# Kernel tuning notes

Measured on AMD Instinct MI355X. Metric: run time of the kernel, lower is better.

The kernel has to match this reference:

```python
import jax, jax.numpy as jnp
import numpy as np

NTYPES = 4
RCUT = 6.0
MIXED_TYPES = False
BOX = 40.0  # Angstrom, sets realistic atomic density


def setup_inputs() -> dict:
    key = jax.random.key(0)
    k1, k2 = jax.random.split(key)
    nframes, nloc = 2, 4096
    coord = jax.random.uniform(k1, (nframes, nloc * 3), dtype=jnp.float32) * BOX
    atype = jax.random.randint(k2, (nframes, nloc), 0, NTYPES, dtype=jnp.int32)
    return {"coord": coord, "atype": atype}


def reference(coord, atype):
    # cell=None branch: extended coords == local coords, nall == nloc
    nframes = coord.shape[0]
    c = coord.reshape(nframes, -1, 3)              # (f, nloc, 3)
    nloc = c.shape[1]
    # diff[f, i, j] = coord[j] - coord[i], shape (f, nloc, nall, 3)
    diff = c[:, None, :, :] - c[:, :, None, :]
    rr2 = jnp.sum(diff * diff, axis=-1)            # (f, nloc, nall)
    # mask self-pairs with inf (torch sets diff rows to inf before squaring)
    eye = jnp.eye(nloc, dtype=bool)
    rr2 = jnp.where(eye[None, :, :], jnp.inf, rr2)
    min_rr2 = jnp.min(rr2, axis=-1)                # (f, nloc)
    mask = rr2 < RCUT ** 2                         # (f, nloc, nall)
    if not MIXED_TYPES:
        # per-type neighbor counts via one-hot contraction (replaces the
        # Python loop over ntypes in the torch code; same math)
        onehot = jax.nn.one_hot(atype, NTYPES, dtype=jnp.int32)  # (f, nall, t)
        nnei = jnp.einsum('fij,fjt->fit', mask.astype(jnp.int32), onehot)
    else:
        valid = (atype >= 0)[:, None, :]
        nnei = jnp.sum(mask & valid, axis=-1).astype(jnp.int32)[..., None]
    max_nnei = jnp.max(nnei, axis=1)               # (f, ntypes) or (f, 1)
    return min_rr2, max_nnei
```

## Files before the change

### kernel.cpp

```cpp
#include <hip/hip_runtime.h>
#include <stdint.h>

#define NFRAMES 2
#define NT 4
#define BLK 256
#define NJ 128
#define JT 32
#define IPT 2
#define FBLK 64

typedef float f32x2 __attribute__((ext_vector_type(2)));

template <bool SELFCHK>
__device__ __forceinline__ void tile_loop(const f32x2* __restrict__ px,
                                          const f32x2* __restrict__ py,
                                          const f32x2* __restrict__ pz,
                                          const uint2* __restrict__ ps,
                                          int jbase,
                                          const int (&ii)[IPT],
                                          const f32x2 (&Xi)[IPT],
                                          const f32x2 (&Yi)[IPT],
                                          const f32x2 (&Zi)[IPT],
                                          float (&mm)[IPT],
                                          unsigned (&cA)[IPT], unsigned (&cB)[IPT]) {
#pragma unroll
    for (int h = 0; h < JT / 2; ++h) {
        const f32x2 jx = px[h], jy = py[h], jz = pz[h];
        const uint2 s2 = ps[h];
        const int j0 = jbase + 2 * h;
#pragma unroll
        for (int k = 0; k < IPT; ++k) {
            f32x2 dx = jx - Xi[k];
            f32x2 dy = jy - Yi[k];
            f32x2 dz = jz - Zi[k];
            f32x2 zz = dz * dz;
            f32x2 t  = __builtin_elementwise_fma(dy, dy, zz);
            f32x2 r2 = __builtin_elementwise_fma(dx, dx, t);
            if (SELFCHK) {
                r2.x = (j0     == ii[k]) ? __builtin_inff() : r2.x;
                r2.y = (j0 + 1 == ii[k]) ? __builtin_inff() : r2.y;
            }
            mm[k] = fminf(mm[k], fminf(r2.x, r2.y));
            cA[k] += (r2.x < 36.0f) ? s2.x : 0u;
            cB[k] += (r2.y < 36.0f) ? s2.y : 0u;
        }
    }
}

__global__ __launch_bounds__(BLK) void ns_pair_kernel(const float* __restrict__ coord,
                                                      const int* __restrict__ atype,
                                                      uint2* __restrict__ part,
                                                      float* __restrict__ out,
                                                      int nloc) {
    const int f = blockIdx.z;
    const int q = nloc / IPT;
    const int ib = blockIdx.y * BLK;
    const int jbase = blockIdx.x * JT;

    if (blockIdx.x == 0 && blockIdx.y == 0 && f == 0 && threadIdx.x < NFRAMES * NT)
        ((unsigned*)out)[(size_t)NFRAMES * nloc + threadIdx.x] = 0u;

    const float* cf = coord + (size_t)f * nloc * 3;
    const int*   tf = atype + (size_t)f * nloc;

    __shared__ float    sx[JT], sy[JT], sz[JT];
    __shared__ unsigned st[JT];
    if (threadIdx.x < JT) {
        const int jl = jbase + threadIdx.x;
        sx[threadIdx.x] = cf[3 * jl];
        sy[threadIdx.x] = cf[3 * jl + 1];
        sz[threadIdx.x] = cf[3 * jl + 2];
        st[threadIdx.x] = 1u << (tf[jl] * 8);
    }
    __syncthreads();

    int ii[IPT];
    f32x2 Xi[IPT], Yi[IPT], Zi[IPT];
    float mm[IPT];
    unsigned cA[IPT], cB[IPT];
    bool ov = false;
#pragma unroll
    for (int k = 0; k < IPT; ++k) {
        const int base = ib + k * q;
        ii[k] = base + threadIdx.x;
        const float x = cf[3 * ii[k]], y = cf[3 * ii[k] + 1], z = cf[3 * ii[k] + 2];
        Xi[k] = (f32x2){x, x};
        Yi[k] = (f32x2){y, y};
        Zi[k] = (f32x2){z, z};
        mm[k] = __builtin_inff();
        cA[k] = cB[k] = 0u;
        ov |= (jbase >= base) && (jbase < base + BLK);
    }

    const f32x2* px = (const f32x2*)sx;
    const f32x2* py = (const f32x2*)sy;
    const f32x2* pz = (const f32x2*)sz;
    const uint2* ps = (const uint2*)st;

    if (ov)
        tile_loop<true >(px, py, pz, ps, jbase, ii, Xi, Yi, Zi, mm, cA, cB);
    else
        tile_loop<false>(px, py, pz, ps, jbase, ii, Xi, Yi, Zi, mm, cA, cB);

    const size_t pb = ((size_t)blockIdx.x * NFRAMES + f) * nloc;
#pragma unroll
    for (int k = 0; k < IPT; ++k)
        part[pb + ii[k]] = make_uint2(__float_as_uint(mm[k]), cA[k] + cB[k]);
}

__global__ __launch_bounds__(FBLK) void ns_finalize_kernel(const uint2* __restrict__ part,
                                                           float* __restrict__ out,
                                                           int nloc) {
    const int nbpf = nloc / FBLK;
    const int f = blockIdx.x / nbpf;
    const int i = (blockIdx.x % nbpf) * FBLK + threadIdx.x;

    float ma = __builtin_inff(), mb = __builtin_inff();
    unsigned cacc = 0u, cbacc = 0u;
#pragma unroll 16
    for (int jb = 0; jb < NJ; jb += 2) {
        uint2 va = part[((size_t)jb * NFRAMES + f) * nloc + i];
        uint2 vb = part[((size_t)(jb + 1) * NFRAMES + f) * nloc + i];
        ma = fminf(ma, __uint_as_float(va.x));
        mb = fminf(mb, __uint_as_float(vb.x));
        cacc += va.y;
        cbacc += vb.y;
    }
    out[(size_t)f * nloc + i] = fminf(ma, mb);
    const unsigned c = cacc + cbacc;

    int m0 = (int)(c & 255u);
    int m1 = (int)((c >> 8) & 255u);
    int m2 = (int)((c >> 16) & 255u);
    int m3 = (int)(c >> 24);
    for (int off = 32; off > 0; off >>= 1) {
        m0 = max(m0, __shfl_xor(m0, off, 64));
        m1 = max(m1, __shfl_xor(m1, off, 64));
        m2 = max(m2, __shfl_xor(m2, off, 64));
        m3 = max(m3, __shfl_xor(m3, off, 64));
    }
    if (threadIdx.x < NT) {
        const int t = threadIdx.x;
        const int mv = (t == 0) ? m0 : (t == 1) ? m1 : (t == 2) ? m2 : m3;
        atomicMax((unsigned*)out + (size_t)NFRAMES * nloc + f * NT + t,
                  __float_as_uint((float)mv));
    }
}

extern "C" void kernel_launch(void* const* d_in, const int* in_sizes, int n_in,
                              void* d_out, int out_size, void* d_ws, size_t ws_size,
                              hipStream_t stream) {
    const float* coord = (const float*)d_in[0];
    const int*   atype = (const int*)d_in[1];
    const int nloc = in_sizes[1] / NFRAMES;

    float* out  = (float*)d_out;
    uint2* part = (uint2*)d_ws;

    dim3 grid(NJ, nloc / (BLK * IPT), NFRAMES);
    ns_pair_kernel<<<grid, dim3(BLK), 0, stream>>>(coord, atype, part, out, nloc);

    const int nbpf = nloc / FBLK;
    ns_finalize_kernel<<<NFRAMES * nbpf, FBLK, 0, stream>>>(part, out, nloc);
}
```

Before: 28.03 us.

## Double j-tile width, pack LDS as float4 pairs, use inline packed-FP32 asm

Raises the j-tile from 32 to 64 atoms, halving the number of j-blocks and the partial buffer the finalize kernel reduces. Shared memory now interleaves each j pair into two float4 records (x/y pair and z/type pair), so each step issues two wide LDS reads instead of four narrow ones. The distance math uses inline v_pk_add/mul/fma asm with pre-negated i coordinates, forcing packed FP32 instructions. The unroll drops to 8, and since NJ=64 is hardcoded in the finalize loop, the grid and partial layout must stay consistent.

```diff
diff --git a/kernel.cpp b/kernel.cpp
--- a/kernel.cpp
+++ b/kernel.cpp
@@ -4,45 +4,56 @@
 #define NFRAMES 2
 #define NT 4
 #define BLK 256
-#define NJ 128
-#define JT 32
+#define NJ 64
+#define JT 64
 #define IPT 2
 #define FBLK 64
 
 typedef float f32x2 __attribute__((ext_vector_type(2)));
 
+__device__ __forceinline__ f32x2 pk_r2(f32x2 jx, f32x2 jy, f32x2 jz,
+                                       f32x2 nx, f32x2 ny, f32x2 nz) {
+    f32x2 dx, dy, dz, t1, t2, r2;
+    asm("v_pk_add_f32 %0, %1, %2" : "=v"(dx) : "v"(jx), "v"(nx));
+    asm("v_pk_add_f32 %0, %1, %2" : "=v"(dy) : "v"(jy), "v"(ny));
+    asm("v_pk_add_f32 %0, %1, %2" : "=v"(dz) : "v"(jz), "v"(nz));
+    asm("v_pk_mul_f32 %0, %1, %1" : "=v"(t1) : "v"(dz));
+    asm("v_pk_fma_f32 %0, %1, %1, %2" : "=v"(t2) : "v"(dy), "v"(t1));
+    asm("v_pk_fma_f32 %0, %1, %1, %2" : "=v"(r2) : "v"(dx), "v"(t2));
+    return r2;
+}
+
 template <bool SELFCHK>
-__device__ __forceinline__ void tile_loop(const f32x2* __restrict__ px,
-                                          const f32x2* __restrict__ py,
-                                          const f32x2* __restrict__ pz,
-                                          const uint2* __restrict__ ps,
+__device__ __forceinline__ void tile_loop(const float4* __restrict__ A,
+                                          const float4* __restrict__ B,
                                           int jbase,
                                           const int (&ii)[IPT],
-                                          const f32x2 (&Xi)[IPT],
-                                          const f32x2 (&Yi)[IPT],
-                                          const f32x2 (&Zi)[IPT],
+                                          const f32x2 (&nX)[IPT],
+                                          const f32x2 (&nY)[IPT],
+                                          const f32x2 (&nZ)[IPT],
                                           float (&mm)[IPT],
                                           unsigned (&cA)[IPT], unsigned (&cB)[IPT]) {
-#pragma unroll
+#pragma unroll 8
     for (int h = 0; h < JT / 2; ++h) {
-        const f32x2 jx = px[h], jy = py[h], jz = pz[h];
-        const uint2 s2 = ps[h];
+        const float4 a = A[h];
+        const float4 b = B[h];
+        const f32x2 jx = {a.x, a.y};
+        const f32x2 jy = {a.z, a.w};
+        const f32x2 jz = {b.x, b.y};
+        const unsigned s0 = __float_as_uint(b.z);
+        const unsigned s1 = __float_as_uint(b.w);
         const int j0 = jbase + 2 * h;
 #pragma unroll
         for (int k = 0; k < IPT; ++k) {
-            f32x2 dx = jx - Xi[k];
-            f32x2 dy = jy - Yi[k];
-            f32x2 dz = jz - Zi[k];
-            f32x2 zz = dz * dz;
-            f32x2 t  = __builtin_elementwise_fma(dy, dy, zz);
-            f32x2 r2 = __builtin_elementwise_fma(dx, dx, t);
+            f32x2 r2 = pk_r2(jx, jy, jz, nX[k], nY[k], nZ[k]);
+            float lo = r2.x, hi = r2.y;
             if (SELFCHK) {
-                r2.x = (j0     == ii[k]) ? __builtin_inff() : r2.x;
-                r2.y = (j0 + 1 == ii[k]) ? __builtin_inff() : r2.y;
+                lo = (j0     == ii[k]) ? __builtin_inff() : lo;
+                hi = (j0 + 1 == ii[k]) ? __builtin_inff() : hi;
             }
-            mm[k] = fminf(mm[k], fminf(r2.x, r2.y));
-            cA[k] += (r2.x < 36.0f) ? s2.x : 0u;
-            cB[k] += (r2.y < 36.0f) ? s2.y : 0u;
+            mm[k] = fminf(mm[k], fminf(lo, hi));
+            cA[k] += (lo < 36.0f) ? s0 : 0u;
+            cB[k] += (hi < 36.0f) ? s1 : 0u;
         }
     }
 }
@@ -63,19 +74,19 @@
     const float* cf = coord + (size_t)f * nloc * 3;
     const int*   tf = atype + (size_t)f * nloc;
 
-    __shared__ float    sx[JT], sy[JT], sz[JT];
-    __shared__ unsigned st[JT];
-    if (threadIdx.x < JT) {
-        const int jl = jbase + threadIdx.x;
-        sx[threadIdx.x] = cf[3 * jl];
-        sy[threadIdx.x] = cf[3 * jl + 1];
-        sz[threadIdx.x] = cf[3 * jl + 2];
-        st[threadIdx.x] = 1u << (tf[jl] * 8);
+    __shared__ float4 A[JT / 2], B[JT / 2];
+    if (threadIdx.x < JT / 2) {
+        const int j0 = jbase + 2 * threadIdx.x;
+        A[threadIdx.x] = make_float4(cf[3 * j0], cf[3 * j0 + 3],
+                                     cf[3 * j0 + 1], cf[3 * j0 + 4]);
+        B[threadIdx.x] = make_float4(cf[3 * j0 + 2], cf[3 * j0 + 5],
+                                     __uint_as_float(1u << (tf[j0] * 8)),
+                                     __uint_as_float(1u << (tf[j0 + 1] * 8)));
     }
     __syncthreads();
 
     int ii[IPT];
-    f32x2 Xi[IPT], Yi[IPT], Zi[IPT];
+    f32x2 nX[IPT], nY[IPT], nZ[IPT];
     float mm[IPT];
     unsigned cA[IPT], cB[IPT];
     bool ov = false;
@@ -83,24 +94,21 @@
     for (int k = 0; k < IPT; ++k) {
         const int base = ib + k * q;
         ii[k] = base + threadIdx.x;
-        const float x = cf[3 * ii[k]], y = cf[3 * ii[k] + 1], z = cf[3 * ii[k] + 2];
-        Xi[k] = (f32x2){x, x};
-        Yi[k] = (f32x2){y, y};
-        Zi[k] = (f32x2){z, z};
+        const float nx = -cf[3 * ii[k]];
+        const float ny = -cf[3 * ii[k] + 1];
+        const float nz = -cf[3 * ii[k] + 2];
+        nX[k] = (f32x2){nx, nx};
+        nY[k] = (f32x2){ny, ny};
+        nZ[k] = (f32x2){nz, nz};
         mm[k] = __builtin_inff();
         cA[k] = cB[k] = 0u;
         ov |= (jbase >= base) && (jbase < base + BLK);
     }
 
-    const f32x2* px = (const f32x2*)sx;
-    const f32x2* py = (const f32x2*)sy;
-    const f32x2* pz = (const f32x2*)sz;
-    const uint2* ps = (const uint2*)st;
-
     if (ov)
-        tile_loop<true >(px, py, pz, ps, jbase, ii, Xi, Yi, Zi, mm, cA, cB);
+        tile_loop<true >(A, B, jbase, ii, nX, nY, nZ, mm, cA, cB);
     else
-        tile_loop<false>(px, py, pz, ps, jbase, ii, Xi, Yi, Zi, mm, cA, cB);
+        tile_loop<false>(A, B, jbase, ii, nX, nY, nZ, mm, cA, cB);
 
     const size_t pb = ((size_t)blockIdx.x * NFRAMES + f) * nloc;
 #pragma unroll
```

Measured after the change: 24.03 us. 1.17x faster.
